# Performance work log

Hardware: AMD Instinct MI355X
Metric: run time of the kernel (lower is better)

Reference implementation:

```python
import jax, jax.numpy as jnp
import numpy as np
from jax import lax

T = 50
THETA = 1.0 - 0.0001  # max_1 - 0.0001, max_1 = T_win/T = 1.0


def conv_t(x, w, b, pad_h):
    # x: [N, C, H, W, T]; slayer conv3d has time-kernel 1 -> conv2d per timestep.
    n, c, h, wd, t = x.shape
    xb = jnp.moveaxis(x, -1, 1).reshape(n * t, c, h, wd)
    y = lax.conv_general_dilated(xb, w, (1, 1), [(pad_h, pad_h), (0, 0)])
    y = y + b[None, :, None, None]
    o, h2, w2 = y.shape[1], y.shape[2], y.shape[3]
    return jnp.moveaxis(y.reshape(n, t, o, h2, w2), 1, -1)


def if_spikes(a):
    # catCuda.getSpikes on an input stacked T times: IF neuron with constant
    # drive a per step, soft reset (v -= theta on spike). a: [N,C,H,W].
    def step(v, _):
        v = v + a
        s = (v >= THETA).astype(a.dtype)
        return v - s * THETA, s
    _, sp = lax.scan(step, jnp.zeros_like(a), None, length=T)
    return jnp.moveaxis(sp, 0, -1)  # [N,C,H,W,T]


def setup_inputs() -> dict:
    key = jax.random.key(0)
    ks = jax.random.split(key, 6)
    def w(k, shape, scale):
        return jax.random.normal(k, shape, jnp.float32) * scale
    x = jax.random.uniform(ks[0], (256, 1, 180, 1, T), jnp.float32)
    return {
        'x': x,
        'w1': w(ks[1], (16, 1, 3, 1), 0.3), 'b1': jnp.zeros(16, jnp.float32),
        'w2': w(ks[2], (32, 16, 9, 1), 0.1), 'b2': jnp.zeros(32, jnp.float32),
        'w3': w(ks[3], (32, 32, 7, 1), 0.1), 'b3': jnp.zeros(32, jnp.float32),
        'wf': w(ks[4], (4, 32, 83, 1), 0.05), 'bf': jnp.zeros(4, jnp.float32),
    }


def reference(x, w1, b1, w2, b2, w3, b3, wf, bf):
    y = conv_t(x, w1, b1, 1)                        # [N,16,180,1,T]
    y = if_spikes(jnp.sum(y, axis=4) / T)           # rate -> spikes
    y = conv_t(y, w2, b2, 1)                        # [N,32,174,1,T]
    y = if_spikes(jnp.sum(y, axis=4) / T)
    y = 1.1 * (y[:, :, 0::2] + y[:, :, 1::2])       # slayer sum-pool (2,1), weight 1.1
    y = if_spikes(jnp.sum(y, axis=4) / T)           # [N,32,87,1,T]
    y = conv_t(y, w3, b3, 1)                        # [N,32,83,1,T]
    y = if_spikes(jnp.sum(y, axis=4) / T)
    out = jnp.einsum('nchwt,ochw->not', y, wf) + bf[None, :, None]  # dense over full spatial
    return jnp.sum(out, axis=-1) / T                # sum_spikes / T -> [N,4]
```

## Files before the change

kernel.cpp:

```cpp
#include <hip/hip_runtime.h>


#define T_STEPS 50
#define THETA   0.9999f

__device__ __forceinline__ float spike_rate(float a) {
    constexpr float INV = 50.0f / 0.9999f;
    float t = a * INV;
    float c = fminf(fmaxf(floorf(t), 0.0f), 50.0f);
    bool risky = (t > 0.5f) && (fabsf(t - rintf(t)) < 5e-4f);
    if (__ballot(risky)) {
        float v = 0.f, cnt = 0.f;
#pragma unroll 1
        for (int k = 0; k < T_STEPS; ++k) {
            v += a;
            float s = (v >= THETA) ? 1.0f : 0.0f;
            v -= s * THETA;
            cnt += s;
        }
        c = cnt;
    }
    return c / 50.0f;
}

extern "C" __global__ void __launch_bounds__(1024)
catnet_kernel(const float* __restrict__ x,
              const float* __restrict__ w1, const float* __restrict__ b1,
              const float* __restrict__ w2, const float* __restrict__ b2,
              const float* __restrict__ w3, const float* __restrict__ b3,
              const float* __restrict__ wf, const float* __restrict__ bf,
              float* __restrict__ out)
{
    const int n    = blockIdx.x;
    const int tid  = threadIdx.x;
    const int wave = tid >> 6;
    const int lane = tid & 63;

    __shared__ float xbar[182];
    __shared__ float r1e[16][91];
    __shared__ float r1o[16][91];
    __shared__ float r3p[32][89];
    __shared__ float r4s[32][83];
    __shared__ float part[16];

    if (tid < 16)              { r1e[tid][0] = 0.f; r1o[tid][90] = 0.f; }
    if (tid >= 32 && tid < 64) { r3p[tid-32][0] = 0.f; r3p[tid-32][88] = 0.f; }
    if (tid == 64)             { xbar[0] = 0.f; xbar[181] = 0.f; }

    const float* xn = x + (size_t)n * (180 * 50);
    if (tid < 720) {
        const int h = tid >> 2, q = tid & 3;
        const float2* row = (const float2*)(xn + h * 50);
        float s = 0.f;
        for (int k = q; k < 25; k += 4) {
            float2 v = row[k];
            s += v.x + v.y;
        }
        s += __shfl_xor(s, 1, 4);
        s += __shfl_xor(s, 2, 4);
        if (q == 0) xbar[h + 1] = s;
    }
    __syncthreads();

    for (int idx = tid; idx < 16 * 180; idx += 1024) {
        int c = idx / 180, h = idx - c * 180;
        float a = w1[c*3+0] * xbar[h] + w1[c*3+1] * xbar[h+1] + w1[c*3+2] * xbar[h+2];
        a = a / 50.0f + b1[c];
        float r = spike_rate(a);
        int pidx = h + 1;
        float* dst = (pidx & 1) ? &r1o[c][pidx >> 1] : &r1e[c][pidx >> 1];
        *dst = r;
    }
    __syncthreads();

    {
        const int g   = __builtin_amdgcn_readfirstlane(tid >> 7);
        const int p   = tid & 127;
        const bool act = p < 87;
        const int pr  = act ? p : 0;
        const float* wb = w2 + g * 4 * 144;

        float a0[4], a1[4];
#pragma unroll
        for (int j = 0; j < 4; ++j) { a0[j] = b2[g*4 + j]; a1[j] = a0[j]; }

#pragma unroll 2
        for (int ci = 0; ci < 16; ++ci) {
            float we[5], wo[5];
#pragma unroll
            for (int d = 0; d < 5; ++d) {
                we[d] = r1e[ci][pr + d];
                wo[d] = r1o[ci][pr + d];
            }
#pragma unroll
            for (int j = 0; j < 4; ++j) {
                const float* wj = wb + j * 144 + ci * 9;
                a0[j] += wj[0]*we[0] + wj[1]*wo[0] + wj[2]*we[1] + wj[3]*wo[1]
                       + wj[4]*we[2] + wj[5]*wo[2] + wj[6]*we[3] + wj[7]*wo[3]
                       + wj[8]*we[4];
                a1[j] += wj[0]*wo[0] + wj[1]*we[1] + wj[2]*wo[1] + wj[3]*we[2]
                       + wj[4]*wo[2] + wj[5]*we[3] + wj[6]*wo[3] + wj[7]*we[4]
                       + wj[8]*wo[4];
            }
        }
#pragma unroll
        for (int j = 0; j < 4; ++j) {
            float r20 = spike_rate(a0[j]);
            float r21 = spike_rate(a1[j]);
            float r3  = spike_rate(1.1f * (r20 + r21));
            if (act) r3p[g*4 + j][p + 1] = r3;
        }
    }
    __syncthreads();

    {
        const int g4   = __builtin_amdgcn_readfirstlane((wave >> 1) * 4);
        const int half = wave & 1;
        const int cnt  = half ? 41 : 42;
        const bool act = lane < cnt;
        const int h0   = half * 42 + lane;
        const int hr   = act ? h0 : 0;
        const float* wb = w3 + g4 * 224;

        float a[4];
#pragma unroll
        for (int j = 0; j < 4; ++j) a[j] = b3[g4 + j];

#pragma unroll 2
        for (int ci = 0; ci < 32; ++ci) {
            float rv[7];
#pragma unroll
            for (int kh = 0; kh < 7; ++kh) rv[kh] = r3p[ci][hr + kh];
#pragma unroll
            for (int j = 0; j < 4; ++j) {
                const float* wj = wb + j * 224 + ci * 7;
#pragma unroll
                for (int kh = 0; kh < 7; ++kh)
                    a[j] += wj[kh] * rv[kh];
            }
        }
#pragma unroll
        for (int j = 0; j < 4; ++j) {
            float r = spike_rate(a[j]);
            if (act) r4s[g4 + j][h0] = r;
        }
    }
    __syncthreads();

    {
        const int o = wave >> 2, q = wave & 3;
        const float* r4f = &r4s[0][0];
        const float* wo  = wf + o * (32 * 83);
        float acc = 0.f;
        for (int j = q * 64 + lane; j < 32 * 83; j += 256)
            acc += r4f[j] * wo[j];
#pragma unroll
        for (int off = 32; off > 0; off >>= 1)
            acc += __shfl_down(acc, off, 64);
        if (lane == 0) part[wave] = acc;
    }
    __syncthreads();
    if (tid < 4) {
        float s = part[tid*4] + part[tid*4+1] + part[tid*4+2] + part[tid*4+3];
        out[n * 4 + tid] = s + bf[tid];
    }
}

extern "C" void kernel_launch(void* const* d_in, const int* in_sizes, int n_in,
                              void* d_out, int out_size, void* d_ws, size_t ws_size,
                              hipStream_t stream) {
    const float* x  = (const float*)d_in[0];
    const float* w1 = (const float*)d_in[1];
    const float* b1 = (const float*)d_in[2];
    const float* w2 = (const float*)d_in[3];
    const float* b2 = (const float*)d_in[4];
    const float* w3 = (const float*)d_in[5];
    const float* b3 = (const float*)d_in[6];
    const float* wf = (const float*)d_in[7];
    const float* bf = (const float*)d_in[8];
    float* outp = (float*)d_out;

    catnet_kernel<<<dim3(256), dim3(1024), 0, stream>>>(
        x, w1, b1, w2, b2, w3, b3, wf, bf, outp);
}
```

Before: 104.9 us.

## Split each sample across two 512-thread blocks with atomic output accumulation

Each sample is now handled by two blocks of 512 threads instead of one 1024-thread block. Each block recomputes the input reduction and the first layer, then computes its own half of the spatial positions for the later convolution stages, including an overlapping halo. The final dense-layer partial sums are combined with atomicAdd into an output that is zeroed by a preceding memset. The goal is more, shorter blocks and better lane use in the convolution stages. The cost is redundant first-layer work, atomics, and an extra memset launch.

```diff
diff --git a/kernel.cpp b/kernel.cpp
--- a/kernel.cpp
+++ b/kernel.cpp
@@ -23,7 +23,7 @@
     return c / 50.0f;
 }
 
-extern "C" __global__ void __launch_bounds__(1024)
+extern "C" __global__ void __launch_bounds__(512)
 catnet_kernel(const float* __restrict__ x,
               const float* __restrict__ w1, const float* __restrict__ b1,
               const float* __restrict__ w2, const float* __restrict__ b2,
@@ -31,7 +31,9 @@
               const float* __restrict__ wf, const float* __restrict__ bf,
               float* __restrict__ out)
 {
-    const int n    = blockIdx.x;
+    const int bid  = blockIdx.x;
+    const int n    = bid >> 1;
+    const int s    = bid & 1;
     const int tid  = threadIdx.x;
     const int wave = tid >> 6;
     const int lane = tid & 63;
@@ -41,28 +43,26 @@
     __shared__ float r1o[16][91];
     __shared__ float r3p[32][89];
     __shared__ float r4s[32][83];
-    __shared__ float part[16];
 
     if (tid < 16)              { r1e[tid][0] = 0.f; r1o[tid][90] = 0.f; }
     if (tid >= 32 && tid < 64) { r3p[tid-32][0] = 0.f; r3p[tid-32][88] = 0.f; }
     if (tid == 64)             { xbar[0] = 0.f; xbar[181] = 0.f; }
 
     const float* xn = x + (size_t)n * (180 * 50);
-    if (tid < 720) {
-        const int h = tid >> 2, q = tid & 3;
+    if (tid < 360) {
+        const int h = tid >> 1, q = tid & 1;
         const float2* row = (const float2*)(xn + h * 50);
-        float s = 0.f;
-        for (int k = q; k < 25; k += 4) {
+        float sv = 0.f;
+        for (int k = q; k < 25; k += 2) {
             float2 v = row[k];
-            s += v.x + v.y;
+            sv += v.x + v.y;
         }
-        s += __shfl_xor(s, 1, 4);
-        s += __shfl_xor(s, 2, 4);
-        if (q == 0) xbar[h + 1] = s;
+        sv += __shfl_xor(sv, 1, 2);
+        if (q == 0) xbar[h + 1] = sv;
     }
     __syncthreads();
 
-    for (int idx = tid; idx < 16 * 180; idx += 1024) {
+    for (int idx = tid; idx < 16 * 180; idx += 512) {
         int c = idx / 180, h = idx - c * 180;
         float a = w1[c*3+0] * xbar[h] + w1[c*3+1] * xbar[h+1] + w1[c*3+2] * xbar[h+2];
         a = a / 50.0f + b1[c];
@@ -74,10 +74,11 @@
     __syncthreads();
 
     {
-        const int g   = __builtin_amdgcn_readfirstlane(tid >> 7);
-        const int p   = tid & 127;
-        const bool act = p < 87;
-        const int pr  = act ? p : 0;
+        const int g    = __builtin_amdgcn_readfirstlane(wave);
+        const int cntp = s ? 46 : 47;
+        const int pbase= s ? 41 : 0;
+        const bool act = lane < cntp;
+        const int p    = pbase + (act ? lane : 0);
         const float* wb = w2 + g * 4 * 144;
 
         float a0[4], a1[4];
@@ -89,8 +90,8 @@
             float we[5], wo[5];
 #pragma unroll
             for (int d = 0; d < 5; ++d) {
-                we[d] = r1e[ci][pr + d];
-                wo[d] = r1o[ci][pr + d];
+                we[d] = r1e[ci][p + d];
+                wo[d] = r1o[ci][p + d];
             }
 #pragma unroll
             for (int j = 0; j < 4; ++j) {
@@ -114,12 +115,11 @@
     __syncthreads();
 
     {
-        const int g4   = __builtin_amdgcn_readfirstlane((wave >> 1) * 4);
-        const int half = wave & 1;
-        const int cnt  = half ? 41 : 42;
-        const bool act = lane < cnt;
-        const int h0   = half * 42 + lane;
-        const int hr   = act ? h0 : 0;
+        const int g4   = __builtin_amdgcn_readfirstlane(wave) * 4;
+        const int cnth = s ? 41 : 42;
+        const int hbase= s ? 42 : 0;
+        const bool act = lane < cnth;
+        const int h0   = hbase + (act ? lane : 0);
         const float* wb = w3 + g4 * 224;
 
         float a[4];
@@ -130,7 +130,7 @@
         for (int ci = 0; ci < 32; ++ci) {
             float rv[7];
 #pragma unroll
-            for (int kh = 0; kh < 7; ++kh) rv[kh] = r3p[ci][hr + kh];
+            for (int kh = 0; kh < 7; ++kh) rv[kh] = r3p[ci][h0 + kh];
 #pragma unroll
             for (int j = 0; j < 4; ++j) {
                 const float* wj = wb + j * 224 + ci * 7;
@@ -147,22 +147,25 @@
     }
     __syncthreads();
 
-    {
-        const int o = wave >> 2, q = wave & 3;
-        const float* r4f = &r4s[0][0];
-        const float* wo  = wf + o * (32 * 83);
+    if (wave < 4) {
+        const int o    = __builtin_amdgcn_readfirstlane(wave);
+        const int cnth = s ? 41 : 42;
+        const int hbase= s ? 42 : 0;
+        const bool act = lane < cnth;
+        const int hh   = hbase + (act ? lane : 0);
         float acc = 0.f;
-        for (int j = q * 64 + lane; j < 32 * 83; j += 256)
-            acc += r4f[j] * wo[j];
+        for (int c = 0; c < 32; ++c) {
+            float rv = act ? r4s[c][hh] : 0.f;
+            float wv = act ? wf[(o * 32 + c) * 83 + hh] : 0.f;
+            acc += rv * wv;
+        }
 #pragma unroll
         for (int off = 32; off > 0; off >>= 1)
             acc += __shfl_down(acc, off, 64);
-        if (lane == 0) part[wave] = acc;
-    }
-    __syncthreads();
-    if (tid < 4) {
-        float s = part[tid*4] + part[tid*4+1] + part[tid*4+2] + part[tid*4+3];
-        out[n * 4 + tid] = s + bf[tid];
+        if (lane == 0) {
+            float contrib = s ? (acc + bf[o]) : acc;
+            atomicAdd(&out[n * 4 + o], contrib);
+        }
     }
 }
 
@@ -180,6 +183,8 @@
     const float* bf = (const float*)d_in[8];
     float* outp = (float*)d_out;
 
-    catnet_kernel<<<dim3(256), dim3(1024), 0, stream>>>(
+    hipMemsetAsync(outp, 0, (size_t)out_size * sizeof(float), stream);
+
+    catnet_kernel<<<dim3(512), dim3(512), 0, stream>>>(
         x, w1, b1, w2, b2, w3, b3, wf, bf, outp);
 }
```

After: 111.8 us. +6.5%, slower.

## Split fused per-sample kernel into four stage kernels through workspace buffers

Applied to the files above, without the earlier changes.

Replaces the single 1024-thread-per-sample fused kernel with four kernels (conv1, conv2+pool, conv3, dense) that pass intermediates through global workspace. The conv stages get 2048 small blocks instead of 256, spreading work across more CUs and avoiding block-wide barriers between stages. In exchange it adds three extra launches and global-memory round trips for the intermediates, and it falls back to the fused kernel when the workspace is too small.

```diff
diff --git a/kernel.cpp b/kernel.cpp
--- a/kernel.cpp
+++ b/kernel.cpp
@@ -23,6 +23,151 @@
     return c / 50.0f;
 }
 
+#define R1_PER_N   (16 * 91)
+#define R1_TOTAL   (256 * R1_PER_N)
+#define R3_PER_N   (32 * 89)
+#define R3_TOTAL   (256 * R3_PER_N)
+#define R4_PER_N   (32 * 83)
+#define R4_TOTAL   (256 * R4_PER_N)
+
+extern "C" __global__ void __launch_bounds__(512)
+k1_conv1(const float* __restrict__ x, const float* __restrict__ w1,
+         const float* __restrict__ b1,
+         float* __restrict__ r1e, float* __restrict__ r1o)
+{
+    const int n = blockIdx.x;
+    const int tid = threadIdx.x;
+    __shared__ float xbar[182];
+    if (tid == 448) { xbar[0] = 0.f; xbar[181] = 0.f; }
+    if (tid >= 464 && tid < 480) r1e[(n * 16 + (tid - 464)) * 91 + 0]  = 0.f;
+    if (tid >= 480 && tid < 496) r1o[(n * 16 + (tid - 480)) * 91 + 90] = 0.f;
+
+    const float* xn = x + (size_t)n * (180 * 50);
+    if (tid < 360) {
+        const int h = tid >> 1, q = tid & 1;
+        const float2* row = (const float2*)(xn + h * 50);
+        float sv = 0.f;
+        for (int k = q; k < 25; k += 2) { float2 v = row[k]; sv += v.x + v.y; }
+        sv += __shfl_xor(sv, 1, 2);
+        if (q == 0) xbar[h + 1] = sv;
+    }
+    __syncthreads();
+
+    for (int idx = tid; idx < 16 * 180; idx += 512) {
+        int c = idx / 180, h = idx - c * 180;
+        float a = w1[c*3+0] * xbar[h] + w1[c*3+1] * xbar[h+1] + w1[c*3+2] * xbar[h+2];
+        a = a / 50.0f + b1[c];
+        float r = spike_rate(a);
+        int pidx = h + 1;
+        if (pidx & 1) r1o[(n * 16 + c) * 91 + (pidx >> 1)] = r;
+        else          r1e[(n * 16 + c) * 91 + (pidx >> 1)] = r;
+    }
+}
+
+extern "C" __global__ void __launch_bounds__(128)
+k2_conv2pool(const float* __restrict__ r1e, const float* __restrict__ r1o,
+             const float* __restrict__ w2, const float* __restrict__ b2,
+             float* __restrict__ r3)
+{
+    const int n = blockIdx.x;
+    const int g = blockIdx.y;
+    const int p0 = threadIdx.x;
+    const bool act = p0 < 87;
+    const int p = act ? p0 : 0;
+    const float* wb = w2 + g * 4 * 144;
+    const float* r1eb = r1e + n * R1_PER_N;
+    const float* r1ob = r1o + n * R1_PER_N;
+
+    float a0[4], a1[4];
+#pragma unroll
+    for (int j = 0; j < 4; ++j) { a0[j] = b2[g*4 + j]; a1[j] = a0[j]; }
+
+#pragma unroll 2
+    for (int ci = 0; ci < 16; ++ci) {
+        float we[5], wo[5];
+#pragma unroll
+        for (int d = 0; d < 5; ++d) {
+            we[d] = r1eb[ci * 91 + p + d];
+            wo[d] = r1ob[ci * 91 + p + d];
+        }
+#pragma unroll
+        for (int j = 0; j < 4; ++j) {
+            const float* wj = wb + j * 144 + ci * 9;
+            a0[j] += wj[0]*we[0] + wj[1]*wo[0] + wj[2]*we[1] + wj[3]*wo[1]
+                   + wj[4]*we[2] + wj[5]*wo[2] + wj[6]*we[3] + wj[7]*wo[3]
+                   + wj[8]*we[4];
+            a1[j] += wj[0]*wo[0] + wj[1]*we[1] + wj[2]*wo[1] + wj[3]*we[2]
+                   + wj[4]*wo[2] + wj[5]*we[3] + wj[6]*wo[3] + wj[7]*we[4]
+                   + wj[8]*wo[4];
+        }
+    }
+#pragma unroll
+    for (int j = 0; j < 4; ++j) {
+        float r20 = spike_rate(a0[j]);
+        float r21 = spike_rate(a1[j]);
+        float r3v = spike_rate(1.1f * (r20 + r21));
+        if (act) {
+            float* dst = r3 + (size_t)(n * 32 + g * 4 + j) * 89;
+            dst[p + 1] = r3v;
+            if (p0 == 0) { dst[0] = 0.f; dst[88] = 0.f; }
+        }
+    }
+}
+
+extern "C" __global__ void __launch_bounds__(128)
+k3_conv3(const float* __restrict__ r3, const float* __restrict__ w3,
+         const float* __restrict__ b3, float* __restrict__ r4)
+{
+    const int n = blockIdx.x;
+    const int g4 = blockIdx.y * 4;
+    const int h0 = threadIdx.x;
+    const bool act = h0 < 83;
+    const int h = act ? h0 : 0;
+    const float* wb = w3 + g4 * 224;
+    const float* r3b = r3 + (size_t)n * R3_PER_N;
+
+    float a[4];
+#pragma unroll
+    for (int j = 0; j < 4; ++j) a[j] = b3[g4 + j];
+
+#pragma unroll 2
+    for (int ci = 0; ci < 32; ++ci) {
+        float rv[7];
+#pragma unroll
+        for (int kh = 0; kh < 7; ++kh) rv[kh] = r3b[ci * 89 + h + kh];
+#pragma unroll
+        for (int j = 0; j < 4; ++j) {
+            const float* wj = wb + j * 224 + ci * 7;
+#pragma unroll
+            for (int kh = 0; kh < 7; ++kh)
+                a[j] += wj[kh] * rv[kh];
+        }
+    }
+#pragma unroll
+    for (int j = 0; j < 4; ++j) {
+        float r = spike_rate(a[j]);
+        if (act) r4[(size_t)(n * 32 + g4 + j) * 83 + h] = r;
+    }
+}
+
+extern "C" __global__ void __launch_bounds__(256)
+k4_dense(const float* __restrict__ r4, const float* __restrict__ wf,
+         const float* __restrict__ bf, float* __restrict__ out)
+{
+    const int n = blockIdx.x;
+    const int o = threadIdx.x >> 6;
+    const int lane = threadIdx.x & 63;
+    const float* r4n = r4 + (size_t)n * R4_PER_N;
+    const float* wo  = wf + o * R4_PER_N;
+    float acc = 0.f;
+    for (int j = lane; j < R4_PER_N; j += 64)
+        acc += r4n[j] * wo[j];
+#pragma unroll
+    for (int off = 32; off > 0; off >>= 1)
+        acc += __shfl_down(acc, off, 64);
+    if (lane == 0) out[n * 4 + o] = acc + bf[o];
+}
+
 extern "C" __global__ void __launch_bounds__(1024)
 catnet_kernel(const float* __restrict__ x,
               const float* __restrict__ w1, const float* __restrict__ b1,
@@ -52,10 +197,7 @@
         const int h = tid >> 2, q = tid & 3;
         const float2* row = (const float2*)(xn + h * 50);
         float s = 0.f;
-        for (int k = q; k < 25; k += 4) {
-            float2 v = row[k];
-            s += v.x + v.y;
-        }
+        for (int k = q; k < 25; k += 4) { float2 v = row[k]; s += v.x + v.y; }
         s += __shfl_xor(s, 1, 4);
         s += __shfl_xor(s, 2, 4);
         if (q == 0) xbar[h + 1] = s;
@@ -88,10 +230,7 @@
         for (int ci = 0; ci < 16; ++ci) {
             float we[5], wo[5];
 #pragma unroll
-            for (int d = 0; d < 5; ++d) {
-                we[d] = r1e[ci][pr + d];
-                wo[d] = r1o[ci][pr + d];
-            }
+            for (int d = 0; d < 5; ++d) { we[d] = r1e[ci][pr + d]; wo[d] = r1o[ci][pr + d]; }
 #pragma unroll
             for (int j = 0; j < 4; ++j) {
                 const float* wj = wb + j * 144 + ci * 9;
@@ -118,8 +257,7 @@
         const int half = wave & 1;
         const int cnt  = half ? 41 : 42;
         const bool act = lane < cnt;
-        const int h0   = half * 42 + lane;
-        const int hr   = act ? h0 : 0;
+        const int h0   = half * 42 + (act ? lane : 0);
         const float* wb = w3 + g4 * 224;
 
         float a[4];
@@ -130,13 +268,12 @@
         for (int ci = 0; ci < 32; ++ci) {
             float rv[7];
 #pragma unroll
-            for (int kh = 0; kh < 7; ++kh) rv[kh] = r3p[ci][hr + kh];
+            for (int kh = 0; kh < 7; ++kh) rv[kh] = r3p[ci][h0 + kh];
 #pragma unroll
             for (int j = 0; j < 4; ++j) {
                 const float* wj = wb + j * 224 + ci * 7;
 #pragma unroll
-                for (int kh = 0; kh < 7; ++kh)
-                    a[j] += wj[kh] * rv[kh];
+                for (int kh = 0; kh < 7; ++kh) a[j] += wj[kh] * rv[kh];
             }
         }
 #pragma unroll
@@ -180,6 +317,18 @@
     const float* bf = (const float*)d_in[8];
     float* outp = (float*)d_out;
 
-    catnet_kernel<<<dim3(256), dim3(1024), 0, stream>>>(
-        x, w1, b1, w2, b2, w3, b3, wf, bf, outp);
-}
+    const size_t need = (size_t)(2 * R1_TOTAL + R3_TOTAL + R4_TOTAL) * sizeof(float);
+    if (ws_size >= need) {
+        float* r1e = (float*)d_ws;
+        float* r1o = r1e + R1_TOTAL;
+        float* r3  = r1o + R1_TOTAL;
+        float* r4  = r3  + R3_TOTAL;
+        k1_conv1   <<<dim3(256),    dim3(512), 0, stream>>>(x, w1, b1, r1e, r1o);
+        k2_conv2pool<<<dim3(256, 8), dim3(128), 0, stream>>>(r1e, r1o, w2, b2, r3);
+        k3_conv3   <<<dim3(256, 8), dim3(128), 0, stream>>>(r3, w3, b3, r4);
+        k4_dense   <<<dim3(256),    dim3(256), 0, stream>>>(r4, wf, bf, outp);
+    } else {
+        catnet_kernel<<<dim3(256), dim3(1024), 0, stream>>>(
+            x, w1, b1, w2, b2, w3, b3, wf, bf, outp);
+    }
+}
```

New measurement: 131.1 us. 1.25x slower.
